# Performance work log

Hardware: AMD Instinct MI355X
Metric: run time of the kernel (lower is better)

Reference implementation:

```python
import jax, jax.numpy as jnp
import numpy as np

B, T, C, H, DH, L, V = 16, 1023, 384, 6, 64, 6, 256
FF = 4 * C
EPS = 1e-5


def _ln(x, g, b):
    mu = x.mean(-1, keepdims=True)
    var = ((x - mu) ** 2).mean(-1, keepdims=True)
    return (x - mu) * jax.lax.rsqrt(var + EPS) * g + b


def setup_inputs() -> dict:
    key = jax.random.key(0)
    ks = jax.random.split(key, 12)
    n = lambda k, shp: jax.random.normal(k, shp, dtype=jnp.float32) * 0.02
    return {
        "x": jax.random.randint(ks[0], (B, T), 0, V),
        "targets": jax.random.randint(ks[1], (B, T), 0, V),
        "tok_emb": n(ks[2], (V, C)),
        "pos_emb": n(ks[3], (T, C)),
        "Wq": n(ks[4], (L, C, C)), "Wk": n(ks[5], (L, C, C)), "Wv": n(ks[6], (L, C, C)),
        "Wo": n(ks[7], (L, C, C)), "bo": jnp.zeros((L, C)),
        "ln1_g": jnp.ones((L, C)), "ln1_b": jnp.zeros((L, C)),
        "ln2_g": jnp.ones((L, C)), "ln2_b": jnp.zeros((L, C)),
        "W1": n(ks[8], (L, C, FF)), "b1": jnp.zeros((L, FF)),
        "W2": n(ks[9], (L, FF, C)), "b2": jnp.zeros((L, C)),
        "lnf_g": jnp.ones((C,)), "lnf_b": jnp.zeros((C,)),
        "Wf": n(ks[10], (C, V)), "bf": jnp.zeros((V,)),
    }


def _forward(x, targets, tok_emb, pos_emb, Wq, Wk, Wv, Wo, bo,
             ln1_g, ln1_b, ln2_g, ln2_b, W1, b1, W2, b2, lnf_g, lnf_b, Wf, bf):
    h = tok_emb[x] + pos_emb[None, :, :]  # [B,T,C]
    tril = jnp.tril(jnp.ones((T, T), bool))

    def heads(z, W):  # [B,T,C] @ [C,C] -> [B,H,T,DH]
        return jnp.einsum('btc,cd->btd', z, W).reshape(B, T, H, DH).transpose(0, 2, 1, 3)

    def layer(h, p):
        wq, wk, wv, wo, bo_, g1, be1, g2, be2, w1, bb1, w2, bb2 = p
        z = _ln(h, g1, be1)
        q, k, v = heads(z, wq), heads(z, wk), heads(z, wv)
        qk = jnp.einsum('bhtd,bhsd->bhts', q, k) * (DH ** -0.5)
        zm = jnp.where(tril, qk, 0.0)
        # faithful to torch: masked_fill_(zeromask == 0, -inf)
        zm = jnp.where(zm == 0.0, -jnp.inf, zm)
        att = jax.nn.softmax(zm, axis=-1)  # dropout = identity (eval)
        o = jnp.einsum('bhts,bhsd->bhtd', att, v).transpose(0, 2, 1, 3).reshape(B, T, C)
        h = h + jnp.einsum('btc,cd->btd', o, wo) + bo_
        z2 = _ln(h, g2, be2)
        ff = jax.nn.relu(jnp.einsum('btc,cf->btf', z2, w1) + bb1)
        h = h + jnp.einsum('btf,fc->btc', ff, w2) + bb2
        return h, None

    params = (Wq, Wk, Wv, Wo, bo, ln1_g, ln1_b, ln2_g, ln2_b, W1, b1, W2, b2)
    h, _ = jax.lax.scan(layer, h, params)
    logits = jnp.einsum('btc,cv->btv', _ln(h, lnf_g, lnf_b), Wf) + bf
    logits2 = logits.reshape(B * T, V)
    logp = jax.nn.log_softmax(logits2, axis=-1)
    loss = -jnp.take_along_axis(logp, targets.reshape(B * T, 1), axis=1).mean()
    return logits2, loss


def reference(x, targets, tok_emb, pos_emb, Wq, Wk, Wv, Wo, bo,
              ln1_g, ln1_b, ln2_g, ln2_b, W1, b1, W2, b2, lnf_g, lnf_b, Wf, bf):
    return _forward(x, targets, tok_emb, pos_emb, Wq, Wk, Wv, Wo, bo,
                    ln1_g, ln1_b, ln2_g, ln2_b, W1, b1, W2, b2, lnf_g, lnf_b, Wf, bf)
```

## Files before the change

### kernel.cpp

```cpp
#include <hip/hip_runtime.h>
#include <hip/hip_bf16.h>
#include <math.h>

#define B_  16
#define T_  1023
#define C_  384
#define H_  6
#define DH_ 64
#define L_  6
#define V_  256
#define FF_ 1536
#define M_  (B_*T_)
#define MP_ 16384
#define EPS_ 1e-5f

typedef __attribute__((ext_vector_type(8))) short bf16x8;
typedef __attribute__((ext_vector_type(4))) short short4v;
typedef __attribute__((ext_vector_type(4))) float f32x4;

__device__ inline short f2bf(float x) {
    union { float f; unsigned u; } c; c.f = x;
    unsigned r = (c.u + 0x7fffu + ((c.u >> 16) & 1u)) >> 16;
    return (short)r;
}

#define GLDS16(g, l) __builtin_amdgcn_global_load_lds(                         \
    (const __attribute__((address_space(1))) void*)(g),                        \
    (__attribute__((address_space(3))) void*)(l), 16, 0, 0)

#define TRRD(dst, va, IMM) asm volatile("ds_read_b64_tr_b16 %0, %1 offset:" IMM \
    : "=v"(dst) : "v"(va))

__global__ void embed_kernel(const int* __restrict__ x, const float* __restrict__ tok,
                             const float* __restrict__ pos, float* __restrict__ h) {
    int i = blockIdx.x * 256 + threadIdx.x;
    if (i >= M_ * C_) return;
    int bt = i / C_;
    int c  = i - bt * C_;
    int t  = bt % T_;
    h[i] = tok[x[bt] * C_ + c] + pos[t * C_ + c];
}

__global__ __launch_bounds__(256) void wconv_kernel(
    const float* __restrict__ Wq, const float* __restrict__ Wk,
    const float* __restrict__ Wv, const float* __restrict__ Wo,
    const float* __restrict__ W1, const float* __restrict__ W2,
    const float* __restrict__ Wf,
    short* __restrict__ qkvt, short* __restrict__ wot, short* __restrict__ w1t,
    short* __restrict__ w2t, short* __restrict__ wft) {
    __shared__ float tile[32][33];
    int t = blockIdx.x;
    const float* src; short* dst; int K, N, tl;
    if (t < 10368) {
        int l = t / 1728, r = t - l * 1728;
        if (r < 432) {
            int which = r / 144; tl = r - which * 144;
            src = (which == 0 ? Wq : which == 1 ? Wk : Wv) + (size_t)l * 384 * 384;
            dst = qkvt + (size_t)l * 1152 * 384 + (size_t)which * 384 * 384;
            K = 384; N = 384;
        } else if (r < 576) {
            tl = r - 432;
            src = Wo + (size_t)l * 384 * 384; dst = wot + (size_t)l * 384 * 384;
            K = 384; N = 384;
        } else if (r < 1152) {
            tl = r - 576;
            src = W1 + (size_t)l * 384 * 1536; dst = w1t + (size_t)l * 1536 * 384;
            K = 384; N = 1536;
        } else {
            tl = r - 1152;
            src = W2 + (size_t)l * 1536 * 384; dst = w2t + (size_t)l * 384 * 1536;
            K = 1536; N = 384;
        }
    } else {
        tl = t - 10368; src = Wf; dst = wft; K = 384; N = 256;
    }
    int ntx = N >> 5;
    int k0 = (tl / ntx) << 5, n0 = (tl % ntx) << 5;
    int rr = threadIdx.x >> 5, cc = threadIdx.x & 31;
#pragma unroll
    for (int p = 0; p < 4; ++p)
        tile[rr + 8 * p][cc] = src[(size_t)(k0 + rr + 8 * p) * N + n0 + cc];
    __syncthreads();
#pragma unroll
    for (int p = 0; p < 4; ++p)
        dst[(size_t)(n0 + rr + 8 * p) * K + k0 + cc] = f2bf(tile[cc][rr + 8 * p]);
}

__global__ __launch_bounds__(512) void qkv_kernel(const float* __restrict__ h,
                                                  const float* __restrict__ lng,
                                                  const float* __restrict__ lnb,
                                                  const short* __restrict__ wt,
                                                  short* __restrict__ outb) {
    __shared__ short Zl[48 * 64 * 8];
    int tid  = threadIdx.x;
    int wave = tid >> 6, lane = tid & 63;
    int g = lane >> 4, r16 = lane & 15;
    int r0 = blockIdx.x * 64;

    const short* wbase = wt + (size_t)(16 * wave + r16) * C_ + 8 * g;
    bf16x8 wf[12];
#pragma unroll
    for (int ks = 0; ks < 12; ++ks) wf[ks] = *(const bf16x8*)(wbase + ks * 32);

    float gv6[6], bv6[6];
#pragma unroll
    for (int i = 0; i < 6; ++i) { gv6[i] = lng[i * 64 + lane]; bv6[i] = lnb[i * 64 + lane]; }

    for (int rr = 0; rr < 8; ++rr) {
        int lrow = 8 * wave + rr;
        const float* rp = h + (size_t)(r0 + lrow) * C_;
        float v[6];
        float s = 0.f, s2 = 0.f;
#pragma unroll
        for (int i = 0; i < 6; ++i) {
            v[i] = rp[i * 64 + lane];
            s += v[i]; s2 += v[i] * v[i];
        }
#pragma unroll
        for (int o = 32; o > 0; o >>= 1) {
            s  += __shfl_xor(s,  o, 64);
            s2 += __shfl_xor(s2, o, 64);
        }
        float mu = s * (1.0f / C_);
        float rs = rsqrtf(s2 * (1.0f / C_) - mu * mu + EPS_);
#pragma unroll
        for (int i = 0; i < 6; ++i) {
            int col = i * 64 + lane;
            Zl[(col >> 3) * 512 + lrow * 8 + (col & 7)] =
                f2bf((v[i] - mu) * rs * gv6[i] + bv6[i]);
        }
    }
    __syncthreads();

    for (int c = 0; c < 9; ++c) {
        f32x4 acc[4];
#pragma unroll
        for (int mj = 0; mj < 4; ++mj) { acc[mj][0]=0.f; acc[mj][1]=0.f; acc[mj][2]=0.f; acc[mj][3]=0.f; }
#pragma unroll
        for (int ks = 0; ks < 12; ++ks) {
#pragma unroll
            for (int mj = 0; mj < 4; ++mj) {
                bf16x8 bz = *(const bf16x8*)(Zl + ((4 * ks + g) * 64 + 16 * mj + r16) * 8);
                acc[mj] = __builtin_amdgcn_mfma_f32_16x16x32_bf16(wf[ks], bz, acc[mj], 0, 0, 0);
            }
        }
        if (c + 1 < 9) {
#pragma unroll
            for (int ks = 0; ks < 12; ++ks)
                wf[ks] = *(const bf16x8*)(wbase + (size_t)(c + 1) * 128 * C_ + ks * 32);
        }
#pragma unroll
        for (int mj = 0; mj < 4; ++mj) {
            short4v ov;
#pragma unroll
            for (int rg = 0; rg < 4; ++rg) ov[rg] = f2bf(acc[mj][rg]);
            *(short4v*)(outb + (size_t)(r0 + 16 * mj + r16) * 1152
                        + 128 * c + 16 * wave + 4 * g) = ov;
        }
    }
}

__global__ __launch_bounds__(512) void wo_kernel(const short* __restrict__ ob,
                                                 const short* __restrict__ wt,
                                                 const float* __restrict__ bo,
                                                 float* __restrict__ h,
                                                 const float* __restrict__ lng,
                                                 const float* __restrict__ lnb,
                                                 short* __restrict__ zout) {
    __shared__ short Ol[48 * 64 * 8];
    int tid  = threadIdx.x;
    int wave = tid >> 6, lane = tid & 63;
    int g = lane >> 4, r16 = lane & 15;
    int r0 = blockIdx.x * 64;

    {
        const short* go = ob + (size_t)(r0 + lane) * C_ + wave * 8;
        short* lo = Ol + (wave * 64 + lane) * 8;
#pragma unroll
        for (int ro = 0; ro < 6; ++ro) { GLDS16(go, lo); go += 64; lo += 4096; }
    }

    const short* wbase = wt + (size_t)(48 * wave + r16) * C_ + 8 * g;
    bf16x8 wf[12];
#pragma unroll
    for (int ks2 = 0; ks2 < 4; ++ks2)
#pragma unroll
        for (int j = 0; j < 3; ++j)
            wf[ks2 * 3 + j] = *(const bf16x8*)(wbase + (size_t)(16 * j) * C_ + 32 * ks2);

    asm volatile("s_waitcnt vmcnt(0)" ::: "memory");
    __builtin_amdgcn_s_barrier();
    asm volatile("" ::: "memory");

    f32x4 acc[4][3];
#pragma unroll
    for (int mi = 0; mi < 4; ++mi)
#pragma unroll
        for (int j = 0; j < 3; ++j) { acc[mi][j][0]=0.f; acc[mi][j][1]=0.f; acc[mi][j][2]=0.f; acc[mi][j][3]=0.f; }

    for (int kc = 0; kc < 3; ++kc) {
#pragma unroll
        for (int ks2 = 0; ks2 < 4; ++ks2) {
            bf16x8 pa[4];
#pragma unroll
            for (int mi = 0; mi < 4; ++mi)
                pa[mi] = *(const bf16x8*)(Ol + ((16 * kc + 4 * ks2 + g) * 64 + 16 * mi + r16) * 8);
#pragma unroll
            for (int j = 0; j < 3; ++j)
#pragma unroll
                for (int mi = 0; mi < 4; ++mi)
                    acc[mi][j] = __builtin_amdgcn_mfma_f32_16x16x32_bf16(pa[mi], wf[ks2 * 3 + j], acc[mi][j], 0, 0, 0);
        }
        if (kc + 1 < 3) {
#pragma unroll
            for (int ks2 = 0; ks2 < 4; ++ks2)
#pragma unroll
                for (int j = 0; j < 3; ++j)
                    wf[ks2 * 3 + j] = *(const bf16x8*)(wbase + (size_t)(16 * j) * C_
                                                       + 128 * (kc + 1) + 32 * ks2);
        }
    }
    __syncthreads();

    float rsum[4][4], rsq[4][4];
#pragma unroll
    for (int mi = 0; mi < 4; ++mi)
#pragma unroll
        for (int rg = 0; rg < 4; ++rg) { rsum[mi][rg] = 0.f; rsq[mi][rg] = 0.f; }

#pragma unroll
    for (int j = 0; j < 3; ++j) {
        int col = 48 * wave + 16 * j + r16;
        float bj = bo[col];
#pragma unroll
        for (int mi = 0; mi < 4; ++mi) {
#pragma unroll
            for (int rg = 0; rg < 4; ++rg) {
                int row = r0 + 16 * mi + 4 * g + rg;
                float hv = h[(size_t)row * C_ + col] + acc[mi][j][rg] + bj;
                h[(size_t)row * C_ + col] = hv;
                acc[mi][j][rg] = hv;
                rsum[mi][rg] += hv;
                rsq[mi][rg]  += hv * hv;
            }
        }
    }
#pragma unroll
    for (int o = 1; o < 16; o <<= 1) {
#pragma unroll
        for (int mi = 0; mi < 4; ++mi)
#pragma unroll
            for (int rg = 0; rg < 4; ++rg) {
                rsum[mi][rg] += __shfl_xor(rsum[mi][rg], o, 64);
                rsq[mi][rg]  += __shfl_xor(rsq[mi][rg],  o, 64);
            }
    }
    float* St = (float*)Ol;
    if (r16 == 0) {
#pragma unroll
        for (int mi = 0; mi < 4; ++mi)
#pragma unroll
            for (int rg = 0; rg < 4; ++rg) {
                int rr = 16 * mi + 4 * g + rg;
                St[rr * 16 + 2 * wave]     = rsum[mi][rg];
                St[rr * 16 + 2 * wave + 1] = rsq[mi][rg];
            }
    }
    __syncthreads();
    if (tid < 64) {
        float s = 0.f, s2 = 0.f;
#pragma unroll
        for (int w = 0; w < 8; ++w) { s += St[tid * 16 + 2 * w]; s2 += St[tid * 16 + 2 * w + 1]; }
        float mu  = s * (1.0f / C_);
        float var = s2 * (1.0f / C_) - mu * mu;
        St[tid * 16]     = mu;
        St[tid * 16 + 1] = rsqrtf(var + EPS_);
    }
    __syncthreads();
#pragma unroll
    for (int j = 0; j < 3; ++j) {
        int col = 48 * wave + 16 * j + r16;
        float gam = lng[col], bet = lnb[col];
#pragma unroll
        for (int mi = 0; mi < 4; ++mi) {
#pragma unroll
            for (int rg = 0; rg < 4; ++rg) {
                int rr = 16 * mi + 4 * g + rg;
                float mu = St[rr * 16], rs = St[rr * 16 + 1];
                zout[(size_t)(r0 + rr) * C_ + col] = f2bf((acc[mi][j][rg] - mu) * rs * gam + bet);
            }
        }
    }
}

__global__ __launch_bounds__(512) void ffn_kernel(const short* __restrict__ z,
                                                  const short* __restrict__ w1t,
                                                  const short* __restrict__ w2t,
                                                  const float* __restrict__ b1,
                                                  const float* __restrict__ b2,
                                                  float* __restrict__ h) {
    __shared__ short Zl[48 * 64 * 8];
    __shared__ short Pl[16 * 64 * 8];
    int tid  = threadIdx.x;
    int wave = tid >> 6, lane = tid & 63;
    int g = lane >> 4, r16 = lane & 15;
    int r0 = blockIdx.x * 64;

    {
        const short* gz = z + (size_t)(r0 + lane) * C_ + wave * 8;
        short* lz = Zl + (wave * 64 + lane) * 8;
#pragma unroll
        for (int ro = 0; ro < 6; ++ro) {
            GLDS16(gz, lz);
            gz += 64;
            lz += 8 * 64 * 8;
        }
    }

    const short* w1base = w1t + (size_t)(16 * wave + r16) * C_ + 8 * g;
    const short* w2base = w2t + (size_t)(48 * wave + r16) * FF_ + 8 * g;

    bf16x8 w1f[12];
#pragma unroll
    for (int ks = 0; ks < 12; ++ks)
        w1f[ks] = *(const bf16x8*)(w1base + ks * 32);

    asm volatile("s_waitcnt vmcnt(0)" ::: "memory");
    __builtin_amdgcn_s_barrier();
    asm volatile("" ::: "memory");

    f32x4 acc2[4][3];
#pragma unroll
    for (int mi = 0; mi < 4; ++mi)
#pragma unroll
        for (int j = 0; j < 3; ++j) { acc2[mi][j][0]=0.f; acc2[mi][j][1]=0.f; acc2[mi][j][2]=0.f; acc2[mi][j][3]=0.f; }

    for (int c = 0; c < 12; ++c) {
        bf16x8 w2f[12];
#pragma unroll
        for (int ks2 = 0; ks2 < 4; ++ks2)
#pragma unroll
            for (int j = 0; j < 3; ++j)
                w2f[ks2 * 3 + j] = *(const bf16x8*)(w2base + (size_t)(16 * j) * FF_
                                                    + 128 * c + 32 * ks2);

        f32x4 acc1[4];
#pragma unroll
        for (int mj = 0; mj < 4; ++mj) { acc1[mj][0]=0.f; acc1[mj][1]=0.f; acc1[mj][2]=0.f; acc1[mj][3]=0.f; }
#pragma unroll
        for (int ks = 0; ks < 12; ++ks) {
#pragma unroll
            for (int mj = 0; mj < 4; ++mj) {
                bf16x8 bz = *(const bf16x8*)(Zl + ((4 * ks + g) * 64 + 16 * mj + r16) * 8);
                acc1[mj] = __builtin_amdgcn_mfma_f32_16x16x32_bf16(w1f[ks], bz, acc1[mj], 0, 0, 0);
            }
        }
        f32x4 b1v = *(const f32x4*)(b1 + 128 * c + 16 * wave + 4 * g);
        int oct = 2 * wave + (g >> 1);
#pragma unroll
        for (int mj = 0; mj < 4; ++mj) {
            short4v pv;
#pragma unroll
            for (int rg = 0; rg < 4; ++rg)
                pv[rg] = f2bf(fmaxf(acc1[mj][rg] + b1v[rg], 0.f));
            *(short4v*)(Pl + (oct * 64 + 16 * mj + r16) * 8 + (g & 1) * 4) = pv;
        }
        __syncthreads();

        if (c + 1 < 12) {
#pragma unroll
            for (int ks = 0; ks < 12; ++ks)
                w1f[ks] = *(const bf16x8*)(w1base + (size_t)(c + 1) * 128 * C_ + ks * 32);
        }

#pragma unroll
        for (int ks2 = 0; ks2 < 4; ++ks2) {
            bf16x8 pa[4];
#pragma unroll
            for (int mi = 0; mi < 4; ++mi)
                pa[mi] = *(const bf16x8*)(Pl + ((4 * ks2 + g) * 64 + 16 * mi + r16) * 8);
#pragma unroll
            for (int j = 0; j < 3; ++j) {
#pragma unroll
                for (int mi = 0; mi < 4; ++mi)
                    acc2[mi][j] = __builtin_amdgcn_mfma_f32_16x16x32_bf16(pa[mi], w2f[ks2 * 3 + j], acc2[mi][j], 0, 0, 0);
            }
        }
        __syncthreads();
    }

#pragma unroll
    for (int j = 0; j < 3; ++j) {
        int col = 48 * wave + 16 * j + r16;
        float bj = b2[col];
#pragma unroll
        for (int mi = 0; mi < 4; ++mi) {
#pragma unroll
            for (int rg = 0; rg < 4; ++rg) {
                int row = r0 + 16 * mi + 4 * g + rg;
                h[(size_t)row * C_ + col] += acc2[mi][j][rg] + bj;
            }
        }
    }
}

__global__ __launch_bounds__(512) void final_kernel(const float* __restrict__ h,
                                                    const float* __restrict__ lng,
                                                    const float* __restrict__ lnb,
                                                    const short* __restrict__ wt,
                                                    const float* __restrict__ bf,
                                                    const int* __restrict__ tgt,
                                                    float* __restrict__ logits,
                                                    float* __restrict__ nll) {
    __shared__ short Zl[48 * 64 * 8];
    __shared__ float Lg[64][260];
    int tid  = threadIdx.x;
    int wave = tid >> 6, lane = tid & 63;
    int g = lane >> 4, r16 = lane & 15;
    int r0 = blockIdx.x * 64;

    const short* wbase = wt + (size_t)(16 * wave + r16) * C_ + 8 * g;
    bf16x8 wf[12];
#pragma unroll
    for (int ks = 0; ks < 12; ++ks) wf[ks] = *(const bf16x8*)(wbase + ks * 32);

    float gv6[6], bv6[6];
#pragma unroll
    for (int i = 0; i < 6; ++i) { gv6[i] = lng[i * 64 + lane]; bv6[i] = lnb[i * 64 + lane]; }

    for (int rr = 0; rr < 8; ++rr) {
        int lrow = 8 * wave + rr;
        const float* rp = h + (size_t)(r0 + lrow) * C_;
        float v[6];
        float s = 0.f, s2 = 0.f;
#pragma unroll
        for (int i = 0; i < 6; ++i) {
            v[i] = rp[i * 64 + lane];
            s += v[i]; s2 += v[i] * v[i];
        }
#pragma unroll
        for (int o = 32; o > 0; o >>= 1) {
            s  += __shfl_xor(s,  o, 64);
            s2 += __shfl_xor(s2, o, 64);
        }
        float mu = s * (1.0f / C_);
        float rs = rsqrtf(s2 * (1.0f / C_) - mu * mu + EPS_);
#pragma unroll
        for (int i = 0; i < 6; ++i) {
            int col = i * 64 + lane;
            Zl[(col >> 3) * 512 + lrow * 8 + (col & 7)] =
                f2bf((v[i] - mu) * rs * gv6[i] + bv6[i]);
        }
    }
    __syncthreads();

    for (int c = 0; c < 2; ++c) {
        f32x4 acc[4];
#pragma unroll
        for (int mj = 0; mj < 4; ++mj) { acc[mj][0]=0.f; acc[mj][1]=0.f; acc[mj][2]=0.f; acc[mj][3]=0.f; }
#pragma unroll
        for (int ks = 0; ks < 12; ++ks) {
#pragma unroll
            for (int mj = 0; mj < 4; ++mj) {
                bf16x8 bz = *(const bf16x8*)(Zl + ((4 * ks + g) * 64 + 16 * mj + r16) * 8);
                acc[mj] = __builtin_amdgcn_mfma_f32_16x16x32_bf16(wf[ks], bz, acc[mj], 0, 0, 0);
            }
        }
        if (c + 1 < 2) {
#pragma unroll
            for (int ks = 0; ks < 12; ++ks)
                wf[ks] = *(const bf16x8*)(wbase + (size_t)128 * C_ + ks * 32);
        }
        int colb = 128 * c + 16 * wave + 4 * g;
        f32x4 bv4 = *(const f32x4*)(bf + colb);
#pragma unroll
        for (int mj = 0; mj < 4; ++mj) {
            int lrow = 16 * mj + r16;
            int row  = r0 + lrow;
            f32x4 ov;
#pragma unroll
            for (int rg = 0; rg < 4; ++rg) {
                ov[rg] = acc[mj][rg] + bv4[rg];
                Lg[lrow][colb + rg] = ov[rg];
            }
            if (row < M_) *(f32x4*)(logits + (size_t)row * V_ + colb) = ov;
        }
    }
    __syncthreads();

    for (int rr = 0; rr < 8; ++rr) {
        int lrow = 8 * wave + rr;
        int row  = r0 + lrow;
        float v[4];
        float mx = -INFINITY;
#pragma unroll
        for (int i = 0; i < 4; ++i) {
            v[i] = Lg[lrow][i * 64 + lane];
            mx = fmaxf(mx, v[i]);
        }
#pragma unroll
        for (int o = 32; o > 0; o >>= 1) mx = fmaxf(mx, __shfl_xor(mx, o, 64));
        float s = 0.f;
#pragma unroll
        for (int i = 0; i < 4; ++i) s += expf(v[i] - mx);
#pragma unroll
        for (int o = 32; o > 0; o >>= 1) s += __shfl_xor(s, o, 64);
        if (lane == 0 && row < M_) {
            float lse = mx + logf(s);
            nll[row] = lse - Lg[lrow][tgt[row]];
        }
    }
}

__device__ __forceinline__ void attn_step(int kt, int qg, int g, int r16,
                                          const char* Kb, unsigned ka, unsigned va,
                                          short (*Pw)[40],
                                          bf16x8 qf0, bf16x8 qf1,
                                          f32x4* o_acc, float& m, float& l) {
    f32x4 s0, s1;
    s0[0]=0.f;s0[1]=0.f;s0[2]=0.f;s0[3]=0.f;
    s1[0]=0.f;s1[1]=0.f;s1[2]=0.f;s1[3]=0.f;
    bf16x8 a00 = *(const bf16x8*)(Kb + ka);
    bf16x8 a01 = *(const bf16x8*)(Kb + (ka ^ 64u));
    bf16x8 a10 = *(const bf16x8*)(Kb + ka + 2048u);
    bf16x8 a11 = *(const bf16x8*)(Kb + ((ka + 2048u) ^ 64u));
    s0 = __builtin_amdgcn_mfma_f32_16x16x32_bf16(a00, qf0, s0, 0, 0, 0);
    s0 = __builtin_amdgcn_mfma_f32_16x16x32_bf16(a01, qf1, s0, 0, 0, 0);
    s1 = __builtin_amdgcn_mfma_f32_16x16x32_bf16(a10, qf0, s1, 0, 0, 0);
    s1 = __builtin_amdgcn_mfma_f32_16x16x32_bf16(a11, qf1, s1, 0, 0, 0);

    int kb0 = kt * 32 + 4 * g;
    float sv[8];
#pragma unroll
    for (int r = 0; r < 4; ++r) {
        sv[r]     = (kb0 + r      <= qg) ? s0[r] * 0.125f : -3e38f;
        sv[4 + r] = (kb0 + 16 + r <= qg) ? s1[r] * 0.125f : -3e38f;
    }
    float pmax = sv[0];
#pragma unroll
    for (int i = 1; i < 8; ++i) pmax = fmaxf(pmax, sv[i]);
    pmax = fmaxf(pmax, __shfl_xor(pmax, 16, 64));
    pmax = fmaxf(pmax, __shfl_xor(pmax, 32, 64));
    float mn   = fmaxf(m, pmax);
    float corr = __expf(m - mn);
    float rs = 0.f;
    short pb[8];
#pragma unroll
    for (int i = 0; i < 8; ++i) {
        float p = __expf(sv[i] - mn);
        rs += p;
        pb[i] = f2bf(p);
    }
    rs += __shfl_xor(rs, 16, 64);
    rs += __shfl_xor(rs, 32, 64);
    l = l * corr + rs;
    m = mn;

    short4v t0w, t1w;
    t0w[0]=pb[0]; t0w[1]=pb[1]; t0w[2]=pb[2]; t0w[3]=pb[3];
    t1w[0]=pb[4]; t1w[1]=pb[5]; t1w[2]=pb[6]; t1w[3]=pb[7];
    *(short4v*)&Pw[r16][4 * g]      = t0w;
    *(short4v*)&Pw[r16][16 + 4 * g] = t1w;

    short4v v0, v1, v2, v3, v4, v5, v6, v7;
    TRRD(v0, va, "0");    TRRD(v1, va, "512");
    TRRD(v2, va, "128");  TRRD(v3, va, "640");
    TRRD(v4, va, "256");  TRRD(v5, va, "768");
    TRRD(v6, va, "384");  TRRD(v7, va, "896");

    bf16x8 pB = *(const bf16x8*)&Pw[r16][8 * g];
#pragma unroll
    for (int d = 0; d < 4; ++d) {
        o_acc[d][0] *= corr; o_acc[d][1] *= corr;
        o_acc[d][2] *= corr; o_acc[d][3] *= corr;
    }
    asm volatile("s_waitcnt lgkmcnt(0)" ::: "memory");
    __builtin_amdgcn_sched_barrier(0);

    bf16x8 av0, av1, av2, av3;
#pragma unroll
    for (int i = 0; i < 4; ++i) {
        av0[i] = v0[i]; av0[i + 4] = v1[i];
        av1[i] = v2[i]; av1[i + 4] = v3[i];
        av2[i] = v4[i]; av2[i + 4] = v5[i];
        av3[i] = v6[i]; av3[i + 4] = v7[i];
    }
    o_acc[0] = __builtin_amdgcn_mfma_f32_16x16x32_bf16(av0, pB, o_acc[0], 0, 0, 0);
    o_acc[1] = __builtin_amdgcn_mfma_f32_16x16x32_bf16(av1, pB, o_acc[1], 0, 0, 0);
    o_acc[2] = __builtin_amdgcn_mfma_f32_16x16x32_bf16(av2, pB, o_acc[2], 0, 0, 0);
    o_acc[3] = __builtin_amdgcn_mfma_f32_16x16x32_bf16(av3, pB, o_acc[3], 0, 0, 0);
}

__global__ __launch_bounds__(256) void attn_kernel(const short* __restrict__ qkv,
                                                   short* __restrict__ o) {
    __shared__ short Kl[2][32 * 64];
    __shared__ short Vl[2][32 * 64];
    __shared__ short P_lds[4][16][40];

    int tid  = threadIdx.x;
    int wave = tid >> 6;
    int lane = tid & 63;
    int g    = lane >> 4;
    int r16  = lane & 15;

    int qtA = blockIdx.x;
    int qtB = 15 - qtA;
    int bh = blockIdx.y;
    int b  = bh / H_, hh = bh - b * H_;
    size_t rbase = (size_t)b * T_;
    int qoff = hh * 64;

    int q0A = qtA * 64, q0B = qtB * 64;
    int qgA = q0A + wave * 16 + r16;
    int qgB = q0B + wave * 16 + r16;

    const short* qrA = qkv + (rbase + qgA) * 1152 + qoff;
    const short* qrB = qkv + (rbase + qgB) * 1152 + qoff;
    bf16x8 qfA0 = *(const bf16x8*)(qrA + 8 * g);
    bf16x8 qfA1 = *(const bf16x8*)(qrA + 32 + 8 * g);
    bf16x8 qfB0 = *(const bf16x8*)(qrB + 8 * g);
    bf16x8 qfB1 = *(const bf16x8*)(qrB + 32 + 8 * g);

    int kkey = tid >> 3;
    int koct = (tid & 7) ^ (kkey & 7);
    const short* gk = qkv + (rbase + kkey) * 1152 + qoff + 384 + koct * 8;
    int vkey = 4 * (tid >> 5) + ((tid >> 1) & 3);
    int voct = 2 * ((tid >> 3) & 3) + (tid & 1);
    const short* gv = qkv + (rbase + vkey) * 1152 + qoff + 768 + voct * 8;
    short* lk0 = Kl[0] + tid * 8;
    short* lk1 = Kl[1] + tid * 8;
    short* lv0 = Vl[0] + tid * 8;
    short* lv1 = Vl[1] + tid * 8;

    f32x4 oA[4], oB[4];
#pragma unroll
    for (int d = 0; d < 4; ++d) {
        oA[d][0]=0.f; oA[d][1]=0.f; oA[d][2]=0.f; oA[d][3]=0.f;
        oB[d][0]=0.f; oB[d][1]=0.f; oB[d][2]=0.f; oB[d][3]=0.f;
    }
    float mA = -3e38f, lA = 0.f, mB = -3e38f, lB = 0.f;

    const char* Kb0 = (const char*)Kl[0];
    const char* Kb1 = (const char*)Kl[1];
    unsigned ka = (unsigned)(r16 * 128 + ((g ^ (r16 & 7)) << 4));
    unsigned va0 = (unsigned)(size_t)(__attribute__((address_space(3))) short*)Vl[0]
                 + 1024u * (unsigned)g + 8u * (unsigned)r16;
    unsigned va1 = va0 + 4096u;

    int ktA_hi = (q0A + wave * 16 + 15) >> 5;
    int ktB_hi = (q0B + wave * 16 + 15) >> 5;
    int nkt = 2 * (qtB + 1);

    GLDS16(gk, lk0);
    GLDS16(gv, lv0);
    gk += 32 * 1152; gv += 32 * 1152;
    asm volatile("s_waitcnt vmcnt(0)" ::: "memory");
    __builtin_amdgcn_s_barrier();
    asm volatile("" ::: "memory");

    for (int kt = 0; kt < nkt; ++kt) {
        int cur = kt & 1;
        if (kt + 1 < nkt) {
            GLDS16(gk, cur ? lk0 : lk1);
            GLDS16(gv, cur ? lv0 : lv1);
            gk += 32 * 1152; gv += 32 * 1152;
        }
        const char* Kb = cur ? Kb1 : Kb0;
        unsigned va = cur ? va1 : va0;

        if (kt <= ktB_hi)
            attn_step(kt, qgB, g, r16, Kb, ka, va, P_lds[wave], qfB0, qfB1, oB, mB, lB);
        if (kt <= ktA_hi)
            attn_step(kt, qgA, g, r16, Kb, ka, va, P_lds[wave], qfA0, qfA1, oA, mA, lA);

        asm volatile("s_waitcnt vmcnt(0)" ::: "memory");
        __builtin_amdgcn_s_barrier();
        asm volatile("" ::: "memory");
    }

    {
        float inv = (lA > 0.f) ? 1.f / lA : 0.f;
        short* orow = o + (rbase + qgA) * C_ + qoff;
#pragma unroll
        for (int d = 0; d < 4; ++d) {
            short4v ov;
#pragma unroll
            for (int r = 0; r < 4; ++r) ov[r] = f2bf(oA[d][r] * inv);
            *(short4v*)(orow + 16 * d + 4 * g) = ov;
        }
    }
    if (qgB < T_) {
        float inv = (lB > 0.f) ? 1.f / lB : 0.f;
        short* orow = o + (rbase + qgB) * C_ + qoff;
#pragma unroll
        for (int d = 0; d < 4; ++d) {
            short4v ov;
#pragma unroll
            for (int r = 0; r < 4; ++r) ov[r] = f2bf(oB[d][r] * inv);
            *(short4v*)(orow + 16 * d + 4 * g) = ov;
        }
    }
}

__global__ __launch_bounds__(256) void loss_kernel(const float* __restrict__ nll,
                                                   float* __restrict__ loss) {
    __shared__ float sm[256];
    float s = 0.f;
    for (int i = threadIdx.x; i < M_; i += 256) s += nll[i];
    sm[threadIdx.x] = s;
    __syncthreads();
    for (int o = 128; o > 0; o >>= 1) {
        if (threadIdx.x < o) sm[threadIdx.x] += sm[threadIdx.x + o];
        __syncthreads();
    }
    if (threadIdx.x == 0) *loss = sm[0] * (1.0f / M_);
}

extern "C" void kernel_launch(void* const* d_in, const int* in_sizes, int n_in,
                              void* d_out, int out_size, void* d_ws, size_t ws_size,
                              hipStream_t stream) {
    const int*   x       = (const int*)d_in[0];
    const int*   targets = (const int*)d_in[1];
    const float* tok_emb = (const float*)d_in[2];
    const float* pos_emb = (const float*)d_in[3];
    const float* Wq      = (const float*)d_in[4];
    const float* Wk      = (const float*)d_in[5];
    const float* Wv      = (const float*)d_in[6];
    const float* Wo      = (const float*)d_in[7];
    const float* bo      = (const float*)d_in[8];
    const float* ln1_g   = (const float*)d_in[9];
    const float* ln1_b   = (const float*)d_in[10];
    const float* ln2_g   = (const float*)d_in[11];
    const float* ln2_b   = (const float*)d_in[12];
    const float* W1      = (const float*)d_in[13];
    const float* b1      = (const float*)d_in[14];
    const float* W2      = (const float*)d_in[15];
    const float* b2      = (const float*)d_in[16];
    const float* lnf_g   = (const float*)d_in[17];
    const float* lnf_b   = (const float*)d_in[18];
    const float* Wf      = (const float*)d_in[19];
    const float* bf      = (const float*)d_in[20];

    float* logits = (float*)d_out;
    float* loss   = logits + (size_t)M_ * V_;

    float* h    = (float*)d_ws;
    short* z    = (short*)(h + (size_t)MP_ * C_);
    short* big  = z + (size_t)MP_ * C_;
    short* ob   = big + (size_t)MP_ * FF_;
    short* qkvt = ob + (size_t)MP_ * C_;
    short* wot  = qkvt + (size_t)L_ * 1152 * 384;
    short* w1t  = wot + (size_t)L_ * 384 * 384;
    short* w2t  = w1t + (size_t)L_ * 1536 * 384;
    short* wft  = w2t + (size_t)L_ * 1536 * 384;
    float* nll  = (float*)(wft + (size_t)256 * 384);

    wconv_kernel<<<10464, 256, 0, stream>>>(Wq, Wk, Wv, Wo, W1, W2, Wf,
                                            qkvt, wot, w1t, w2t, wft);
    embed_kernel<<<(M_ * C_ + 255) / 256, 256, 0, stream>>>(x, tok_emb, pos_emb, h);

    for (int l = 0; l < L_; ++l) {
        qkv_kernel<<<MP_ / 64, 512, 0, stream>>>(
            h, ln1_g + l * C_, ln1_b + l * C_,
            qkvt + (size_t)l * 1152 * 384, big);
        attn_kernel<<<dim3(8, B_ * H_), 256, 0, stream>>>(big, ob);
        wo_kernel<<<MP_ / 64, 512, 0, stream>>>(
            ob, wot + (size_t)l * 384 * 384, bo + l * C_, h,
            ln2_g + l * C_, ln2_b + l * C_, z);
        ffn_kernel<<<MP_ / 64, 512, 0, stream>>>(
            z, w1t + (size_t)l * 1536 * 384, w2t + (size_t)l * 384 * 1536,
            b1 + l * FF_, b2 + l * C_, h);
    }

    final_kernel<<<MP_ / 64, 512, 0, stream>>>(
        h, lnf_g, lnf_b, wft, bf, targets, logits, nll);
    loss_kernel<<<1, 256, 0, stream>>>(nll, loss);
}
```

Before: 1.211 ms.

## Fuse output projection, LayerNorm2 and FFN into one kernel via LDS

Merges wo_kernel and ffn_kernel into a single wo_ffn_kernel. The LayerNorm2 output is written as bf16 straight into a shared-memory tile in the MFMA operand layout instead of to the global z buffer, and the FFN then runs on that tile in the same block. This removes one global write and read of z per layer plus one kernel launch per layer. In exchange the block now holds Ol, Zl and Pl in LDS at once, roughly 112KB, which likely drops occupancy to one block per CU and adds pressure from preloading the W1 fragments earlier.

```diff
diff --git a/kernel.cpp b/kernel.cpp
--- a/kernel.cpp
+++ b/kernel.cpp
@@ -160,14 +160,19 @@
     }
 }
 
-__global__ __launch_bounds__(512) void wo_kernel(const short* __restrict__ ob,
-                                                 const short* __restrict__ wt,
-                                                 const float* __restrict__ bo,
-                                                 float* __restrict__ h,
-                                                 const float* __restrict__ lng,
-                                                 const float* __restrict__ lnb,
-                                                 short* __restrict__ zout) {
+__global__ __launch_bounds__(512) void wo_ffn_kernel(const short* __restrict__ ob,
+                                                     const short* __restrict__ wot_,
+                                                     const float* __restrict__ bo,
+                                                     float* __restrict__ h,
+                                                     const float* __restrict__ lng,
+                                                     const float* __restrict__ lnb,
+                                                     const short* __restrict__ w1t,
+                                                     const short* __restrict__ w2t,
+                                                     const float* __restrict__ b1,
+                                                     const float* __restrict__ b2) {
     __shared__ short Ol[48 * 64 * 8];
+    __shared__ short Zl[48 * 64 * 8];
+    __shared__ short Pl[16 * 64 * 8];
     int tid  = threadIdx.x;
     int wave = tid >> 6, lane = tid & 63;
     int g = lane >> 4, r16 = lane & 15;
@@ -180,7 +185,7 @@
         for (int ro = 0; ro < 6; ++ro) { GLDS16(go, lo); go += 64; lo += 4096; }
     }
 
-    const short* wbase = wt + (size_t)(48 * wave + r16) * C_ + 8 * g;
+    const short* wbase = wot_ + (size_t)(48 * wave + r16) * C_ + 8 * g;
     bf16x8 wf[12];
 #pragma unroll
     for (int ks2 = 0; ks2 < 4; ++ks2)
@@ -221,6 +226,13 @@
         }
     }
     __syncthreads();
+
+    const short* w1base = w1t + (size_t)(16 * wave + r16) * C_ + 8 * g;
+    const short* w2base = w2t + (size_t)(48 * wave + r16) * FF_ + 8 * g;
+    bf16x8 w1f[12];
+#pragma unroll
+    for (int ks = 0; ks < 12; ++ks)
+        w1f[ks] = *(const bf16x8*)(w1base + ks * 32);
 
     float rsum[4][4], rsq[4][4];
 #pragma unroll
@@ -287,47 +299,12 @@
             for (int rg = 0; rg < 4; ++rg) {
                 int rr = 16 * mi + 4 * g + rg;
                 float mu = St[rr * 16], rs = St[rr * 16 + 1];
-                zout[(size_t)(r0 + rr) * C_ + col] = f2bf((acc[mi][j][rg] - mu) * rs * gam + bet);
-            }
-        }
-    }
-}
-
-__global__ __launch_bounds__(512) void ffn_kernel(const short* __restrict__ z,
-                                                  const short* __restrict__ w1t,
-                                                  const short* __restrict__ w2t,
-                                                  const float* __restrict__ b1,
-                                                  const float* __restrict__ b2,
-                                                  float* __restrict__ h) {
-    __shared__ short Zl[48 * 64 * 8];
-    __shared__ short Pl[16 * 64 * 8];
-    int tid  = threadIdx.x;
-    int wave = tid >> 6, lane = tid & 63;
-    int g = lane >> 4, r16 = lane & 15;
-    int r0 = blockIdx.x * 64;
-
-    {
-        const short* gz = z + (size_t)(r0 + lane) * C_ + wave * 8;
-        short* lz = Zl + (wave * 64 + lane) * 8;
-#pragma unroll
-        for (int ro = 0; ro < 6; ++ro) {
-            GLDS16(gz, lz);
-            gz += 64;
-            lz += 8 * 64 * 8;
-        }
-    }
-
-    const short* w1base = w1t + (size_t)(16 * wave + r16) * C_ + 8 * g;
-    const short* w2base = w2t + (size_t)(48 * wave + r16) * FF_ + 8 * g;
-
-    bf16x8 w1f[12];
-#pragma unroll
-    for (int ks = 0; ks < 12; ++ks)
-        w1f[ks] = *(const bf16x8*)(w1base + ks * 32);
-
-    asm volatile("s_waitcnt vmcnt(0)" ::: "memory");
-    __builtin_amdgcn_s_barrier();
-    asm volatile("" ::: "memory");
+                Zl[(col >> 3) * 512 + rr * 8 + (col & 7)] =
+                    f2bf((acc[mi][j][rg] - mu) * rs * gam + bet);
+            }
+        }
+    }
+    __syncthreads();
 
     f32x4 acc2[4][3];
 #pragma unroll
@@ -764,12 +741,12 @@
             h, ln1_g + l * C_, ln1_b + l * C_,
             qkvt + (size_t)l * 1152 * 384, big);
         attn_kernel<<<dim3(8, B_ * H_), 256, 0, stream>>>(big, ob);
-        wo_kernel<<<MP_ / 64, 512, 0, stream>>>(
+        wo_ffn_kernel<<<MP_ / 64, 512, 0, stream>>>(
             ob, wot + (size_t)l * 384 * 384, bo + l * C_, h,
-            ln2_g + l * C_, ln2_b + l * C_, z);
-        ffn_kernel<<<MP_ / 64, 512, 0, stream>>>(
-            z, w1t + (size_t)l * 1536 * 384, w2t + (size_t)l * 384 * 1536,
-            b1 + l * FF_, b2 + l * C_, h);
+            ln2_g + l * C_, ln2_b + l * C_,
+            w1t + (size_t)l * 1536 * 384, w2t + (size_t)l * 384 * 1536,
+            b1 + l * FF_, b2 + l * C_);
+        ffn_dummy:;
     }
 
     final_kernel<<<MP_ / 64, 512, 0, stream>>>(
```

Result: faster. 1.132 ms (-6.5%).
